# Kernel tuning notes

Measured on AMD Instinct MI355X. Metric: run time of the kernel, lower is better.

The kernel has to match this reference:

```python
import jax, jax.numpy as jnp
import numpy as np

N_LEVELS = 16
F_PER_LEVEL = 2
LOG2_T = 19
TABLE_SIZE = 1 << LOG2_T
BASE_RES = 16
MAX_RES = 4096
GEO_FEAT = 15
N_PTS = 524288

_b = np.exp((np.log(MAX_RES) - np.log(BASE_RES)) / (N_LEVELS - 1))
RES = np.floor(BASE_RES * _b ** np.arange(N_LEVELS)).astype(np.float32)  # [L]
PRIMES = np.array([1, 2654435761, 805459861], dtype=np.uint32)
# 8 trilinear corner offsets
OFFS = np.array([[(i >> 2) & 1, (i >> 1) & 1, i & 1] for i in range(8)], dtype=np.int32)


def hash_encode(x, table):
    # x: [N,3] in [0,1], table: [L,T,F]
    pos = x[None, :, :] * jnp.asarray(RES)[:, None, None]          # [L,N,3]
    p0 = jnp.floor(pos)
    frac = pos - p0                                                 # [L,N,3]
    corners = p0.astype(jnp.uint32)[:, :, None, :] + jnp.asarray(OFFS.astype(np.uint32))  # [L,N,8,3]
    hp = corners * jnp.asarray(PRIMES)                              # uint32 mul (wraps)
    h = (hp[..., 0] ^ hp[..., 1] ^ hp[..., 2]) & jnp.uint32(TABLE_SIZE - 1)  # [L,N,8]
    w = jnp.where(jnp.asarray(OFFS, bool), frac[:, :, None, :], 1.0 - frac[:, :, None, :]).prod(-1)  # [L,N,8]
    feats = jax.vmap(lambda t, i: t[i])(table, h)                   # [L,N,8,F] hashed gather
    out = (w[..., None] * feats).sum(axis=2)                        # [L,N,F]
    return out.transpose(1, 0, 2).reshape(x.shape[0], N_LEVELS * F_PER_LEVEL)  # [N,32]


def setup_inputs() -> dict:
    key = jax.random.key(0)
    ks = jax.random.split(key, 9)
    positions = jax.random.uniform(ks[0], (N_PTS, 3), dtype=jnp.float32)
    aabb = jnp.array([-1.0, -1.0, -1.0, 1.0, 1.0, 1.0], dtype=jnp.float32)
    table = jax.random.uniform(ks[1], (N_LEVELS, TABLE_SIZE, F_PER_LEVEL), minval=-1e-4, maxval=1e-4, dtype=jnp.float32)
    def lin(k, fan_in, fan_out):
        bound = 1.0 / np.sqrt(fan_in)
        kw, kb = jax.random.split(k)
        return (jax.random.uniform(kw, (fan_in, fan_out), minval=-bound, maxval=bound, dtype=jnp.float32),
                jax.random.uniform(kb, (fan_out,), minval=-bound, maxval=bound, dtype=jnp.float32))
    w1, b1 = lin(ks[2], 32, 64)
    w2, b2 = lin(ks[3], 64, 1 + GEO_FEAT)
    hw1, hb1 = lin(ks[4], GEO_FEAT, 64)
    hw2, hb2 = lin(ks[5], 64, 64)
    hw3, hb3 = lin(ks[6], 64, 3)
    return {"positions": positions, "aabb": aabb, "table": table,
            "w1": w1, "b1": b1, "w2": w2, "b2": b2,
            "hw1": hw1, "hb1": hb1, "hw2": hw2, "hb2": hb2, "hw3": hw3, "hb3": hb3}


def reference(positions, aabb, table, w1, b1, w2, b2, hw1, hb1, hw2, hb2, hw3, hb3):
    aabb_min, aabb_max = aabb[:3], aabb[3:]
    x = (positions - aabb_min) / (aabb_max - aabb_min)              # -> [0,1]
    selector = ((x > 0.0) & (x < 1.0)).all(axis=-1)                 # [N]
    enc = hash_encode(x, table)                                     # [N,32]
    h = jax.nn.relu(enc @ w1 + b1)                                  # [N,64]
    base = h @ w2 + b2                                              # [N,16]
    density_before = base[:, :1]
    embedding = base[:, 1:]
    density = jnp.exp(density_before - 1.0) * selector[:, None].astype(base.dtype)  # trunc_exp(x-1)
    hh = jax.nn.relu(embedding @ hw1 + hb1)
    hh = jax.nn.relu(hh @ hw2 + hb2)
    rgb = jax.nn.sigmoid(hh @ hw3 + hb3)                            # [N,3]
    return rgb, density
```

## Files before the change

kernel.cpp:

```cpp
#include <hip/hip_runtime.h>
#include <math.h>

#define NLV 16
#define TBLBITS 19
#define TBLMASK ((1u << TBLBITS) - 1u)
#define P2 2654435761u
#define P3 805459861u

#define D_BASE0 0
#define D_BASE1 4914
#define D_BASE2 18738
#define D_BASE3 58044
#define D_TOTAL 175694

typedef __attribute__((ext_vector_type(8))) short bf16x8;
typedef __attribute__((ext_vector_type(4))) float f32x4;

__device__ __forceinline__ unsigned f2bf(float f) {
    unsigned u = __builtin_bit_cast(unsigned, f);
    return (u + 0x7fffu + ((u >> 16) & 1u)) >> 16;
}

__global__ __launch_bounds__(256)
void dense_repack(const float* __restrict__ table, float* __restrict__ dense)
{
    const int i = blockIdx.x * 256 + threadIdx.x;
    if (i >= D_TOTAL) return;
    int g, lo, dim;
    if (i < 4913)                       { g = 0; lo = i;           dim = 17; }
    else if (i >= D_BASE1 && i < 18738) { g = 1; lo = i - D_BASE1; dim = 24; }
    else if (i >= D_BASE2 && i < 58042) { g = 2; lo = i - D_BASE2; dim = 34; }
    else if (i >= D_BASE3 && i < 175693){ g = 3; lo = i - D_BASE3; dim = 49; }
    else return;
    const unsigned z = (unsigned)lo % (unsigned)dim;
    const unsigned t = (unsigned)lo / (unsigned)dim;
    const unsigned y = t % (unsigned)dim;
    const unsigned x = t / (unsigned)dim;
    const unsigned h = (x ^ y * P2 ^ z * P3) & TBLMASK;
    const float* tl = table + ((size_t)g << 20);
    const float2 v = *reinterpret_cast<const float2*>(tl + ((size_t)h << 1));
    dense[(size_t)i * 2 + 0] = v.x;
    dense[(size_t)i * 2 + 1] = v.y;
}

__global__ __launch_bounds__(256)
void enc_kernel(const float* __restrict__ positions,
                const float* __restrict__ aabb,
                const float* __restrict__ table,
                unsigned* __restrict__ encOut, int npts,
                float r0_, float r1_, float r2_, float r3_,
                float r4_, float r5_, float r6_, float r7_,
                float r8_, float r9_, float r10_, float r11_,
                float r12_, float r13_, float r14_, float r15_)
{
    const unsigned l = blockIdx.y + 4u;
    const unsigned p = blockIdx.x * 256u + threadIdx.x;

    const bool s0 = (l & 1u), s1 = (l & 2u), s2 = (l & 4u), s3 = (l & 8u);
    float a0 = s0 ? r1_  : r0_;
    float a1 = s0 ? r3_  : r2_;
    float a2 = s0 ? r5_  : r4_;
    float a3 = s0 ? r7_  : r6_;
    float a4 = s0 ? r9_  : r8_;
    float a5 = s0 ? r11_ : r10_;
    float a6 = s0 ? r13_ : r12_;
    float a7 = s0 ? r15_ : r14_;
    float c0 = s1 ? a1 : a0;
    float c1 = s1 ? a3 : a2;
    float c2 = s1 ? a5 : a4;
    float c3 = s1 ? a7 : a6;
    float d0 = s2 ? c1 : c0;
    float d1 = s2 ? c3 : c2;
    const float r = s3 ? d1 : d0;

    const float px = positions[p * 3 + 0];
    const float py = positions[p * 3 + 1];
    const float pz = positions[p * 3 + 2];
    const float mnx = aabb[0], mny = aabb[1], mnz = aabb[2];
    const float mxx = aabb[3], mxy = aabb[4], mxz = aabb[5];
    const float x0 = (px - mnx) / (mxx - mnx);
    const float x1 = (py - mny) / (mxy - mny);
    const float x2 = (pz - mnz) / (mxz - mnz);

    const float fx = x0 * r, fy = x1 * r, fz = x2 * r;
    const float gx = floorf(fx), gy = floorf(fy), gz = floorf(fz);
    const unsigned cx = (unsigned)gx, cy = (unsigned)gy, cz = (unsigned)gz;
    const float rx = fx - gx, ry = fy - gy, rz = fz - gz;

    const float* tl = table + ((size_t)l << 20);
    float e0 = 0.f, e1 = 0.f;
    const bool xeven = (cx & 1u) == 0u;

    #pragma unroll
    for (int yz = 0; yz < 4; ++yz) {
        const unsigned dy = (yz >> 1) & 1, dz = yz & 1;
        const unsigned base = ((cy + dy) * P2) ^ ((cz + dz) * P3);
        const float wy = dy ? ry : 1.f - ry;
        const float wz = dz ? rz : 1.f - rz;
        const float wyz = wy * wz;
        const float wa = wyz * (1.f - rx);
        const float wb = wyz * rx;
        const unsigned i0 = (cx ^ base) & TBLMASK;

        float f0x, f0y, f1x, f1y;
        if (xeven) {
            const float4 q = *reinterpret_cast<const float4*>(
                tl + ((size_t)(i0 & ~1u) << 1));
            const bool lo = (i0 & 1u) == 0u;
            f0x = lo ? q.x : q.z;  f0y = lo ? q.y : q.w;
            f1x = lo ? q.z : q.x;  f1y = lo ? q.w : q.y;
        } else {
            const unsigned i1 = ((cx + 1u) ^ base) & TBLMASK;
            const float2 qa = *reinterpret_cast<const float2*>(tl + ((size_t)i0 << 1));
            const float2 qb = *reinterpret_cast<const float2*>(tl + ((size_t)i1 << 1));
            f0x = qa.x; f0y = qa.y; f1x = qb.x; f1y = qb.y;
        }
        e0 = fmaf(wa, f0x, e0); e0 = fmaf(wb, f1x, e0);
        e1 = fmaf(wa, f0y, e1); e1 = fmaf(wb, f1y, e1);
    }
    encOut[(size_t)(l - 4u) * npts + p] = f2bf(e0) | (f2bf(e1) << 16);
}

__global__ __launch_bounds__(256)
void prep_weights(const float* __restrict__ w1, const float* __restrict__ w2,
                  const float* __restrict__ hw1, const float* __restrict__ hw2,
                  const float* __restrict__ hw3, unsigned short* __restrict__ wt)
{
    const int i = blockIdx.x * 256 + threadIdx.x;
    if (i >= 12032) return;
    float v = 0.f;
    if (i < 2560) {
        int n = i / 40, k = i % 40;
        if (k < 32) v = w1[k * 64 + n];
    } else if (i < 5120) {
        int j = i - 2560, n = j / 40, k = j % 40;
        if (k < 15) v = hw1[k * 64 + n];
    } else if (i < 6272) {
        int j = i - 5120, n = j / 72, k = j % 72;
        if (k < 64) v = w2[k * 16 + n];
    } else if (i < 10880) {
        int j = i - 6272, n = j / 72, k = j % 72;
        if (k < 64) v = hw2[k * 64 + n];
    } else {
        int j = i - 10880, n = j / 72, k = j % 72;
        if (k < 64 && n < 3) v = hw3[k * 3 + n];
    }
    wt[i] = (unsigned short)f2bf(v);
}

__device__ __forceinline__ unsigned dense_gather(
    const float* __restrict__ dt, int g, float x0, float x1, float x2)
{
    const float r  = (g & 2) ? ((g & 1) ? 48.f : 33.f) : ((g & 1) ? 23.f : 16.f);
    const int  dim = (g & 2) ? ((g & 1) ? 49 : 34) : ((g & 1) ? 24 : 17);
    const int  bse = (g & 2) ? ((g & 1) ? D_BASE3 : D_BASE2)
                             : ((g & 1) ? D_BASE1 : D_BASE0);
    const float fx = x0 * r, fy = x1 * r, fz = x2 * r;
    const float gx = floorf(fx), gy = floorf(fy), gz = floorf(fz);
    const int cx = (int)gx, cy = (int)gy, cz = (int)gz;
    const float rx = fx - gx, ry = fy - gy, rz = fz - gz;
    float e0 = 0.f, e1 = 0.f;
    #pragma unroll
    for (int xy = 0; xy < 4; ++xy) {
        const int dx = xy >> 1, dy = xy & 1;
        const int row = ((cx + dx) * dim + (cy + dy)) * dim + cz + bse;
        const float wxy = (dx ? rx : 1.f - rx) * (dy ? ry : 1.f - ry);
        const float wa = wxy * (1.f - rz), wb = wxy * rz;
        float f0x, f0y, f1x, f1y;
        if (!(row & 1)) {
            const float4 q = *reinterpret_cast<const float4*>(dt + ((size_t)row << 1));
            f0x = q.x; f0y = q.y; f1x = q.z; f1y = q.w;
        } else {
            const float2 qa = *reinterpret_cast<const float2*>(dt + ((size_t)row << 1));
            const float2 qb = *reinterpret_cast<const float2*>(dt + ((size_t)(row + 1) << 1));
            f0x = qa.x; f0y = qa.y; f1x = qb.x; f1y = qb.y;
        }
        e0 = fmaf(wa, f0x, e0); e0 = fmaf(wb, f1x, e0);
        e1 = fmaf(wa, f0y, e1); e1 = fmaf(wb, f1y, e1);
    }
    return f2bf(e0) | (f2bf(e1) << 16);
}

__global__ __launch_bounds__(256)
void mlp_kernel(const unsigned* __restrict__ enc,
                const unsigned short* __restrict__ wt,
                const float* __restrict__ dense,
                const float* __restrict__ positions,
                const float* __restrict__ aabb,
                const float* __restrict__ b1, const float* __restrict__ b2,
                const float* __restrict__ hb1, const float* __restrict__ hb2,
                const float* __restrict__ hb3,
                float* __restrict__ out, int npts)
{
    __shared__ __align__(16) unsigned short H[4][32 * 72];
    __shared__ float sel_lds[128];

    const int tid  = threadIdx.x;
    const int wave = tid >> 6;
    const int lane = tid & 63;
    const int col  = lane & 15;
    const int lgrp = lane >> 4;
    const int blockPt = blockIdx.x * 128;
    const int wavePt  = blockPt + wave * 32;

    const float mnx = aabb[0], mny = aabb[1], mnz = aabb[2];
    const float mxx = aabb[3], mxy = aabb[4], mxz = aabb[5];

    if (lane < 32) {
        const int gp = wavePt + lane;
        const float px = positions[gp * 3 + 0];
        const float py = positions[gp * 3 + 1];
        const float pz = positions[gp * 3 + 2];
        const float x0 = (px - mnx) / (mxx - mnx);
        const float x1 = (py - mny) / (mxy - mny);
        const float x2 = (pz - mnz) / (mxz - mnz);
        const bool sel = (x0 > 0.f) && (x0 < 1.f) && (x1 > 0.f) && (x1 < 1.f) &&
                         (x2 > 0.f) && (x2 < 1.f);
        sel_lds[wave * 32 + lane] = sel ? 1.f : 0.f;
    }

    float bias1[4], biasH1[4], biasH2[4];
    #pragma unroll
    for (int nt = 0; nt < 4; ++nt) {
        bias1[nt]  = b1[nt * 16 + col];
        biasH1[nt] = hb1[nt * 16 + col];
        biasH2[nt] = hb2[nt * 16 + col];
    }
    const float bias2 = b2[col];
    const float biasH3 = (col < 3) ? hb3[col] : 0.f;

    bf16x8 a1[2];
    #pragma unroll
    for (int mt = 0; mt < 2; ++mt) {
        const int ptl = wavePt + mt * 16 + col;
        const float px = positions[ptl * 3 + 0];
        const float py = positions[ptl * 3 + 1];
        const float pz = positions[ptl * 3 + 2];
        const float x0 = (px - mnx) / (mxx - mnx);
        const float x1 = (py - mny) / (mxy - mny);
        const float x2 = (pz - mnz) / (mxz - mnz);
        const unsigned dv = dense_gather(dense, lgrp, x0, x1, x2);
        const int er = (lgrp == 0) ? 0 : (lgrp * 4 - 4);
        const unsigned e0v = enc[(size_t)(er + 0) * npts + ptl];
        const unsigned e1v = enc[(size_t)(er + 1) * npts + ptl];
        const unsigned e2v = enc[(size_t)(er + 2) * npts + ptl];
        const unsigned e3v = enc[(size_t)(er + 3) * npts + ptl];
        const int cbase = col * 4;
        const unsigned d0 = (unsigned)__builtin_amdgcn_ds_bpermute(cbase,       (int)dv);
        const unsigned d1 = (unsigned)__builtin_amdgcn_ds_bpermute(cbase + 64,  (int)dv);
        const unsigned d2 = (unsigned)__builtin_amdgcn_ds_bpermute(cbase + 128, (int)dv);
        const unsigned d3 = (unsigned)__builtin_amdgcn_ds_bpermute(cbase + 192, (int)dv);
        uint4 v;
        v.x = (lgrp == 0) ? d0 : e0v;
        v.y = (lgrp == 0) ? d1 : e1v;
        v.z = (lgrp == 0) ? d2 : e2v;
        v.w = (lgrp == 0) ? d3 : e3v;
        a1[mt] = __builtin_bit_cast(bf16x8, v);
    }

    const unsigned short* w1t = wt;
    const unsigned short* w3t = wt + 2560;
    const unsigned short* w2t = wt + 5120;
    const unsigned short* w4t = wt + 6272;
    const unsigned short* w5t = wt + 10880;
    unsigned short* Hw = H[wave];

    {
        f32x4 acc[2][4];
        #pragma unroll
        for (int mt = 0; mt < 2; ++mt)
            #pragma unroll
            for (int nt = 0; nt < 4; ++nt) {
                const float b = bias1[nt];
                acc[mt][nt] = (f32x4){b, b, b, b};
            }
        #pragma unroll
        for (int nt = 0; nt < 4; ++nt) {
            const bf16x8 b = *reinterpret_cast<const bf16x8*>(
                w1t + (nt * 16 + col) * 40 + lgrp * 8);
            #pragma unroll
            for (int mt = 0; mt < 2; ++mt)
                acc[mt][nt] = __builtin_amdgcn_mfma_f32_16x16x32_bf16(
                    a1[mt], b, acc[mt][nt], 0, 0, 0);
        }
        #pragma unroll
        for (int mt = 0; mt < 2; ++mt)
            #pragma unroll
            for (int nt = 0; nt < 4; ++nt)
                #pragma unroll
                for (int rr = 0; rr < 4; ++rr) {
                    const float h = fmaxf(acc[mt][nt][rr], 0.f);
                    const int row = mt * 16 + lgrp * 4 + rr;
                    Hw[row * 72 + nt * 16 + col] = (unsigned short)f2bf(h);
                }
    }

    {
        f32x4 acc[2];
        #pragma unroll
        for (int mt = 0; mt < 2; ++mt)
            acc[mt] = (f32x4){bias2, bias2, bias2, bias2};
        #pragma unroll
        for (int ks = 0; ks < 2; ++ks) {
            const bf16x8 b = *reinterpret_cast<const bf16x8*>(
                w2t + col * 72 + ks * 32 + lgrp * 8);
            #pragma unroll
            for (int mt = 0; mt < 2; ++mt) {
                const bf16x8 a = *reinterpret_cast<const bf16x8*>(
                    Hw + (mt * 16 + col) * 72 + ks * 32 + lgrp * 8);
                acc[mt] = __builtin_amdgcn_mfma_f32_16x16x32_bf16(
                    a, b, acc[mt], 0, 0, 0);
            }
        }
        #pragma unroll
        for (int mt = 0; mt < 2; ++mt)
            #pragma unroll
            for (int rr = 0; rr < 4; ++rr) {
                const float base = acc[mt][rr];
                const int row = mt * 16 + lgrp * 4 + rr;
                if (col == 0) {
                    const float dn = __expf(base - 1.f) * sel_lds[wave * 32 + row];
                    out[(size_t)npts * 3 + wavePt + row] = dn;
                } else {
                    Hw[row * 72 + (col - 1)] = (unsigned short)f2bf(base);
                }
            }
        if (lane < 32) {
            const int row = lane;
            Hw[row * 72 + 15] = 0;
            const uint4 z4 = {0, 0, 0, 0};
            *reinterpret_cast<uint4*>(Hw + row * 72 + 16) = z4;
            *reinterpret_cast<uint4*>(Hw + row * 72 + 24) = z4;
        }
    }

    {
        f32x4 acc[2][4];
        #pragma unroll
        for (int mt = 0; mt < 2; ++mt)
            #pragma unroll
            for (int nt = 0; nt < 4; ++nt) {
                const float b = biasH1[nt];
                acc[mt][nt] = (f32x4){b, b, b, b};
            }
        bf16x8 a[2];
        #pragma unroll
        for (int mt = 0; mt < 2; ++mt)
            a[mt] = *reinterpret_cast<const bf16x8*>(
                Hw + (mt * 16 + col) * 72 + lgrp * 8);
        #pragma unroll
        for (int nt = 0; nt < 4; ++nt) {
            const bf16x8 b = *reinterpret_cast<const bf16x8*>(
                w3t + (nt * 16 + col) * 40 + lgrp * 8);
            #pragma unroll
            for (int mt = 0; mt < 2; ++mt)
                acc[mt][nt] = __builtin_amdgcn_mfma_f32_16x16x32_bf16(
                    a[mt], b, acc[mt][nt], 0, 0, 0);
        }
        #pragma unroll
        for (int mt = 0; mt < 2; ++mt)
            #pragma unroll
            for (int nt = 0; nt < 4; ++nt)
                #pragma unroll
                for (int rr = 0; rr < 4; ++rr) {
                    const float h = fmaxf(acc[mt][nt][rr], 0.f);
                    const int row = mt * 16 + lgrp * 4 + rr;
                    Hw[row * 72 + nt * 16 + col] = (unsigned short)f2bf(h);
                }
    }

    {
        f32x4 acc[2][4];
        #pragma unroll
        for (int mt = 0; mt < 2; ++mt)
            #pragma unroll
            for (int nt = 0; nt < 4; ++nt) {
                const float b = biasH2[nt];
                acc[mt][nt] = (f32x4){b, b, b, b};
            }
        #pragma unroll
        for (int ks = 0; ks < 2; ++ks) {
            bf16x8 a[2];
            #pragma unroll
            for (int mt = 0; mt < 2; ++mt)
                a[mt] = *reinterpret_cast<const bf16x8*>(
                    Hw + (mt * 16 + col) * 72 + ks * 32 + lgrp * 8);
            #pragma unroll
            for (int nt = 0; nt < 4; ++nt) {
                const bf16x8 b = *reinterpret_cast<const bf16x8*>(
                    w4t + (nt * 16 + col) * 72 + ks * 32 + lgrp * 8);
                #pragma unroll
                for (int mt = 0; mt < 2; ++mt)
                    acc[mt][nt] = __builtin_amdgcn_mfma_f32_16x16x32_bf16(
                        a[mt], b, acc[mt][nt], 0, 0, 0);
            }
        }
        #pragma unroll
        for (int mt = 0; mt < 2; ++mt)
            #pragma unroll
            for (int nt = 0; nt < 4; ++nt)
                #pragma unroll
                for (int rr = 0; rr < 4; ++rr) {
                    const float h = fmaxf(acc[mt][nt][rr], 0.f);
                    const int row = mt * 16 + lgrp * 4 + rr;
                    Hw[row * 72 + nt * 16 + col] = (unsigned short)f2bf(h);
                }
    }

    {
        f32x4 acc[2];
        #pragma unroll
        for (int mt = 0; mt < 2; ++mt)
            acc[mt] = (f32x4){biasH3, biasH3, biasH3, biasH3};
        #pragma unroll
        for (int ks = 0; ks < 2; ++ks) {
            const bf16x8 b = *reinterpret_cast<const bf16x8*>(
                w5t + col * 72 + ks * 32 + lgrp * 8);
            #pragma unroll
            for (int mt = 0; mt < 2; ++mt) {
                const bf16x8 a = *reinterpret_cast<const bf16x8*>(
                    Hw + (mt * 16 + col) * 72 + ks * 32 + lgrp * 8);
                acc[mt] = __builtin_amdgcn_mfma_f32_16x16x32_bf16(
                    a, b, acc[mt], 0, 0, 0);
            }
        }
        if (col < 3) {
            #pragma unroll
            for (int mt = 0; mt < 2; ++mt)
                #pragma unroll
                for (int rr = 0; rr < 4; ++rr) {
                    const float v = acc[mt][rr];
                    const float rgb = 1.f / (1.f + __expf(-v));
                    const int row = mt * 16 + lgrp * 4 + rr;
                    out[(size_t)(wavePt + row) * 3 + col] = rgb;
                }
        }
    }
}

extern "C" void kernel_launch(void* const* d_in, const int* in_sizes, int n_in,
                              void* d_out, int out_size, void* d_ws, size_t ws_size,
                              hipStream_t stream) {
    const float* positions = (const float*)d_in[0];
    const float* aabb      = (const float*)d_in[1];
    const float* table     = (const float*)d_in[2];
    const float* w1  = (const float*)d_in[3];
    const float* b1  = (const float*)d_in[4];
    const float* w2  = (const float*)d_in[5];
    const float* b2  = (const float*)d_in[6];
    const float* hw1 = (const float*)d_in[7];
    const float* hb1 = (const float*)d_in[8];
    const float* hw2 = (const float*)d_in[9];
    const float* hb2 = (const float*)d_in[10];
    const float* hw3 = (const float*)d_in[11];
    const float* hb3 = (const float*)d_in[12];
    float* out = (float*)d_out;

    const int npts = in_sizes[0] / 3;

    unsigned* encbuf = (unsigned*)d_ws;
    unsigned short* wt = (unsigned short*)((char*)d_ws + (size_t)npts * 12 * 4);
    float* dense = (float*)((char*)d_ws + (size_t)npts * 12 * 4 + 24064);

    float R[NLV];
    const double bb = exp((log(4096.0) - log(16.0)) / 15.0);
    for (int l = 0; l < NLV; ++l)
        R[l] = (float)floor(16.0 * pow(bb, (double)l));

    prep_weights<<<47, 256, 0, stream>>>(w1, w2, hw1, hw2, hw3, wt);
    dense_repack<<<(D_TOTAL + 255) / 256, 256, 0, stream>>>(table, dense);

    dim3 egrid(npts / 256, 12);
    enc_kernel<<<egrid, 256, 0, stream>>>(
        positions, aabb, table, encbuf, npts,
        R[0], R[1], R[2], R[3], R[4], R[5], R[6], R[7],
        R[8], R[9], R[10], R[11], R[12], R[13], R[14], R[15]);

    mlp_kernel<<<npts / 128, 256, 0, stream>>>(
        encbuf, wt, dense, positions, aabb, b1, b2, hb1, hb2, hb3, out, npts);
}
```

Measured before the change: 327.4 us.

## Fuse hash-grid encoding into MLP kernel via shared-memory staging

Measured after the change: 447.5 us. +36.7%, slower.

```diff
diff --git a/kernel.cpp b/kernel.cpp
--- a/kernel.cpp
+++ b/kernel.cpp
@@ -15,6 +15,8 @@
 
 typedef __attribute__((ext_vector_type(8))) short bf16x8;
 typedef __attribute__((ext_vector_type(4))) float f32x4;
+
+struct ResArr { float r[NLV]; };
 
 __device__ __forceinline__ unsigned f2bf(float f) {
     unsigned u = __builtin_bit_cast(unsigned, f);
@@ -41,84 +43,6 @@
     const float2 v = *reinterpret_cast<const float2*>(tl + ((size_t)h << 1));
     dense[(size_t)i * 2 + 0] = v.x;
     dense[(size_t)i * 2 + 1] = v.y;
-}
-
-__global__ __launch_bounds__(256)
-void enc_kernel(const float* __restrict__ positions,
-                const float* __restrict__ aabb,
-                const float* __restrict__ table,
-                unsigned* __restrict__ encOut, int npts,
-                float r0_, float r1_, float r2_, float r3_,
-                float r4_, float r5_, float r6_, float r7_,
-                float r8_, float r9_, float r10_, float r11_,
-                float r12_, float r13_, float r14_, float r15_)
-{
-    const unsigned l = blockIdx.y + 4u;
-    const unsigned p = blockIdx.x * 256u + threadIdx.x;
-
-    const bool s0 = (l & 1u), s1 = (l & 2u), s2 = (l & 4u), s3 = (l & 8u);
-    float a0 = s0 ? r1_  : r0_;
-    float a1 = s0 ? r3_  : r2_;
-    float a2 = s0 ? r5_  : r4_;
-    float a3 = s0 ? r7_  : r6_;
-    float a4 = s0 ? r9_  : r8_;
-    float a5 = s0 ? r11_ : r10_;
-    float a6 = s0 ? r13_ : r12_;
-    float a7 = s0 ? r15_ : r14_;
-    float c0 = s1 ? a1 : a0;
-    float c1 = s1 ? a3 : a2;
-    float c2 = s1 ? a5 : a4;
-    float c3 = s1 ? a7 : a6;
-    float d0 = s2 ? c1 : c0;
-    float d1 = s2 ? c3 : c2;
-    const float r = s3 ? d1 : d0;
-
-    const float px = positions[p * 3 + 0];
-    const float py = positions[p * 3 + 1];
-    const float pz = positions[p * 3 + 2];
-    const float mnx = aabb[0], mny = aabb[1], mnz = aabb[2];
-    const float mxx = aabb[3], mxy = aabb[4], mxz = aabb[5];
-    const float x0 = (px - mnx) / (mxx - mnx);
-    const float x1 = (py - mny) / (mxy - mny);
-    const float x2 = (pz - mnz) / (mxz - mnz);
-
-    const float fx = x0 * r, fy = x1 * r, fz = x2 * r;
-    const float gx = floorf(fx), gy = floorf(fy), gz = floorf(fz);
-    const unsigned cx = (unsigned)gx, cy = (unsigned)gy, cz = (unsigned)gz;
-    const float rx = fx - gx, ry = fy - gy, rz = fz - gz;
-
-    const float* tl = table + ((size_t)l << 20);
-    float e0 = 0.f, e1 = 0.f;
-    const bool xeven = (cx & 1u) == 0u;
-
-    #pragma unroll
-    for (int yz = 0; yz < 4; ++yz) {
-        const unsigned dy = (yz >> 1) & 1, dz = yz & 1;
-        const unsigned base = ((cy + dy) * P2) ^ ((cz + dz) * P3);
-        const float wy = dy ? ry : 1.f - ry;
-        const float wz = dz ? rz : 1.f - rz;
-        const float wyz = wy * wz;
-        const float wa = wyz * (1.f - rx);
-        const float wb = wyz * rx;
-        const unsigned i0 = (cx ^ base) & TBLMASK;
-
-        float f0x, f0y, f1x, f1y;
-        if (xeven) {
-            const float4 q = *reinterpret_cast<const float4*>(
-                tl + ((size_t)(i0 & ~1u) << 1));
-            const bool lo = (i0 & 1u) == 0u;
-            f0x = lo ? q.x : q.z;  f0y = lo ? q.y : q.w;
-            f1x = lo ? q.z : q.x;  f1y = lo ? q.w : q.y;
-        } else {
-            const unsigned i1 = ((cx + 1u) ^ base) & TBLMASK;
-            const float2 qa = *reinterpret_cast<const float2*>(tl + ((size_t)i0 << 1));
-            const float2 qb = *reinterpret_cast<const float2*>(tl + ((size_t)i1 << 1));
-            f0x = qa.x; f0y = qa.y; f1x = qb.x; f1y = qb.y;
-        }
-        e0 = fmaf(wa, f0x, e0); e0 = fmaf(wb, f1x, e0);
-        e1 = fmaf(wa, f0y, e1); e1 = fmaf(wb, f1y, e1);
-    }
-    encOut[(size_t)(l - 4u) * npts + p] = f2bf(e0) | (f2bf(e1) << 16);
 }
 
 __global__ __launch_bounds__(256)
@@ -181,17 +105,18 @@
     return f2bf(e0) | (f2bf(e1) << 16);
 }
 
-__global__ __launch_bounds__(256)
-void mlp_kernel(const unsigned* __restrict__ enc,
-                const unsigned short* __restrict__ wt,
-                const float* __restrict__ dense,
-                const float* __restrict__ positions,
-                const float* __restrict__ aabb,
-                const float* __restrict__ b1, const float* __restrict__ b2,
-                const float* __restrict__ hb1, const float* __restrict__ hb2,
-                const float* __restrict__ hb3,
-                float* __restrict__ out, int npts)
+__global__ __launch_bounds__(256, 4)
+void fused_kernel(const float* __restrict__ positions,
+                  const float* __restrict__ aabb,
+                  const float* __restrict__ table,
+                  const float* __restrict__ dense,
+                  const unsigned short* __restrict__ wt,
+                  const float* __restrict__ b1, const float* __restrict__ b2,
+                  const float* __restrict__ hb1, const float* __restrict__ hb2,
+                  const float* __restrict__ hb3,
+                  float* __restrict__ out, int npts, ResArr R)
 {
+    __shared__ unsigned enc_s[128 * 17];
     __shared__ __align__(16) unsigned short H[4][32 * 72];
     __shared__ float sel_lds[128];
 
@@ -206,18 +131,71 @@
     const float mnx = aabb[0], mny = aabb[1], mnz = aabb[2];
     const float mxx = aabb[3], mxy = aabb[4], mxz = aabb[5];
 
-    if (lane < 32) {
-        const int gp = wavePt + lane;
-        const float px = positions[gp * 3 + 0];
-        const float py = positions[gp * 3 + 1];
-        const float pz = positions[gp * 3 + 2];
+    {
+        const int mypt = tid & 127;
+        const int h = tid >> 7;
+        const float px = positions[(blockPt + mypt) * 3 + 0];
+        const float py = positions[(blockPt + mypt) * 3 + 1];
+        const float pz = positions[(blockPt + mypt) * 3 + 2];
         const float x0 = (px - mnx) / (mxx - mnx);
         const float x1 = (py - mny) / (mxy - mny);
         const float x2 = (pz - mnz) / (mxz - mnz);
-        const bool sel = (x0 > 0.f) && (x0 < 1.f) && (x1 > 0.f) && (x1 < 1.f) &&
-                         (x2 > 0.f) && (x2 < 1.f);
-        sel_lds[wave * 32 + lane] = sel ? 1.f : 0.f;
-    }
+
+        if (h == 0) {
+            const bool sel = (x0 > 0.f) && (x0 < 1.f) && (x1 > 0.f) &&
+                             (x1 < 1.f) && (x2 > 0.f) && (x2 < 1.f);
+            sel_lds[mypt] = sel ? 1.f : 0.f;
+        }
+
+        #pragma unroll
+        for (int j = 0; j < 8; ++j) {
+            unsigned dv;
+            if (j < 2) {
+                dv = dense_gather(dense, 2 * j + h, x0, x1, x2);
+            } else {
+                const float r = h ? R.r[2 * j + 1] : R.r[2 * j];
+                const float fx = x0 * r, fy = x1 * r, fz = x2 * r;
+                const float gx = floorf(fx), gy = floorf(fy), gz = floorf(fz);
+                const unsigned cx = (unsigned)gx, cy = (unsigned)gy, cz = (unsigned)gz;
+                const float rx = fx - gx, ry = fy - gy, rz = fz - gz;
+                const float* tl = table + ((size_t)(2 * j + h) << 20);
+                float e0 = 0.f, e1 = 0.f;
+                const bool xeven = (cx & 1u) == 0u;
+                #pragma unroll
+                for (int yz = 0; yz < 4; ++yz) {
+                    const unsigned dy = (yz >> 1) & 1, dz = yz & 1;
+                    const unsigned base = ((cy + dy) * P2) ^ ((cz + dz) * P3);
+                    const float wy = dy ? ry : 1.f - ry;
+                    const float wz = dz ? rz : 1.f - rz;
+                    const float wyz = wy * wz;
+                    const float wa = wyz * (1.f - rx);
+                    const float wb = wyz * rx;
+                    const unsigned i0 = (cx ^ base) & TBLMASK;
+                    float f0x, f0y, f1x, f1y;
+                    if (xeven) {
+                        const float4 q = *reinterpret_cast<const float4*>(
+                            tl + ((size_t)(i0 & ~1u) << 1));
+                        const bool lo = (i0 & 1u) == 0u;
+                        f0x = lo ? q.x : q.z;  f0y = lo ? q.y : q.w;
+                        f1x = lo ? q.z : q.x;  f1y = lo ? q.w : q.y;
+                    } else {
+                        const unsigned i1 = ((cx + 1u) ^ base) & TBLMASK;
+                        const float2 qa = *reinterpret_cast<const float2*>(
+                            tl + ((size_t)i0 << 1));
+                        const float2 qb = *reinterpret_cast<const float2*>(
+                            tl + ((size_t)i1 << 1));
+                        f0x = qa.x; f0y = qa.y; f1x = qb.x; f1y = qb.y;
+                    }
+                    e0 = fmaf(wa, f0x, e0); e0 = fmaf(wb, f1x, e0);
+                    e1 = fmaf(wa, f0y, e1); e1 = fmaf(wb, f1y, e1);
+                }
+                dv = f2bf(e0) | (f2bf(e1) << 16);
+            }
+            enc_s[mypt * 17 + 2 * j + h] = dv;
+        }
+    }
+
+    __syncthreads();
 
     float bias1[4], biasH1[4], biasH2[4];
     #pragma unroll
@@ -232,29 +210,12 @@
     bf16x8 a1[2];
     #pragma unroll
     for (int mt = 0; mt < 2; ++mt) {
-        const int ptl = wavePt + mt * 16 + col;
-        const float px = positions[ptl * 3 + 0];
-        const float py = positions[ptl * 3 + 1];
-        const float pz = positions[ptl * 3 + 2];
-        const float x0 = (px - mnx) / (mxx - mnx);
-        const float x1 = (py - mny) / (mxy - mny);
-        const float x2 = (pz - mnz) / (mxz - mnz);
-        const unsigned dv = dense_gather(dense, lgrp, x0, x1, x2);
-        const int er = (lgrp == 0) ? 0 : (lgrp * 4 - 4);
-        const unsigned e0v = enc[(size_t)(er + 0) * npts + ptl];
-        const unsigned e1v = enc[(size_t)(er + 1) * npts + ptl];
-        const unsigned e2v = enc[(size_t)(er + 2) * npts + ptl];
-        const unsigned e3v = enc[(size_t)(er + 3) * npts + ptl];
-        const int cbase = col * 4;
-        const unsigned d0 = (unsigned)__builtin_amdgcn_ds_bpermute(cbase,       (int)dv);
-        const unsigned d1 = (unsigned)__builtin_amdgcn_ds_bpermute(cbase + 64,  (int)dv);
-        const unsigned d2 = (unsigned)__builtin_amdgcn_ds_bpermute(cbase + 128, (int)dv);
-        const unsigned d3 = (unsigned)__builtin_amdgcn_ds_bpermute(cbase + 192, (int)dv);
+        const int ptl = wave * 32 + mt * 16 + col;
         uint4 v;
-        v.x = (lgrp == 0) ? d0 : e0v;
-        v.y = (lgrp == 0) ? d1 : e1v;
-        v.z = (lgrp == 0) ? d2 : e2v;
-        v.w = (lgrp == 0) ? d3 : e3v;
+        v.x = enc_s[ptl * 17 + lgrp * 4 + 0];
+        v.y = enc_s[ptl * 17 + lgrp * 4 + 1];
+        v.z = enc_s[ptl * 17 + lgrp * 4 + 2];
+        v.w = enc_s[ptl * 17 + lgrp * 4 + 3];
         a1[mt] = __builtin_bit_cast(bf16x8, v);
     }
 
@@ -458,24 +419,18 @@
 
     const int npts = in_sizes[0] / 3;
 
-    unsigned* encbuf = (unsigned*)d_ws;
-    unsigned short* wt = (unsigned short*)((char*)d_ws + (size_t)npts * 12 * 4);
-    float* dense = (float*)((char*)d_ws + (size_t)npts * 12 * 4 + 24064);
-
-    float R[NLV];
+    unsigned short* wt = (unsigned short*)d_ws;
+    float* dense = (float*)((char*)d_ws + 24064);
+
+    ResArr R;
     const double bb = exp((log(4096.0) - log(16.0)) / 15.0);
     for (int l = 0; l < NLV; ++l)
-        R[l] = (float)floor(16.0 * pow(bb, (double)l));
+        R.r[l] = (float)floor(16.0 * pow(bb, (double)l));
 
     prep_weights<<<47, 256, 0, stream>>>(w1, w2, hw1, hw2, hw3, wt);
     dense_repack<<<(D_TOTAL + 255) / 256, 256, 0, stream>>>(table, dense);
 
-    dim3 egrid(npts / 256, 12);
-    enc_kernel<<<egrid, 256, 0, stream>>>(
-        positions, aabb, table, encbuf, npts,
-        R[0], R[1], R[2], R[3], R[4], R[5], R[6], R[7],
-        R[8], R[9], R[10], R[11], R[12], R[13], R[14], R[15]);
-
-    mlp_kernel<<<npts / 128, 256, 0, stream>>>(
-        encbuf, wt, dense, positions, aabb, b1, b2, hb1, hb2, hb3, out, npts);
-}
+    fused_kernel<<<npts / 128, 256, 0, stream>>>(
+        positions, aabb, table, dense, wt,
+        b1, b2, hb1, hb2, hb3, out, npts, R);
+}
```

## Pipeline encoding and MLP across point chunks in mixed software-pipelined kernel

Applied to the files above, without the earlier changes.

New measurement: 414.7 us. 26.7% more time.

```diff
diff --git a/kernel.cpp b/kernel.cpp
--- a/kernel.cpp
+++ b/kernel.cpp
@@ -12,6 +12,10 @@
 #define D_BASE2 18738
 #define D_BASE3 58044
 #define D_TOTAL 175694
+
+#define WT_OFF    0
+#define DENSE_OFF 24064
+#define ENC_OFF   1429632
 
 typedef __attribute__((ext_vector_type(8))) short bf16x8;
 typedef __attribute__((ext_vector_type(4))) float f32x4;
@@ -41,84 +45,6 @@
     const float2 v = *reinterpret_cast<const float2*>(tl + ((size_t)h << 1));
     dense[(size_t)i * 2 + 0] = v.x;
     dense[(size_t)i * 2 + 1] = v.y;
-}
-
-__global__ __launch_bounds__(256)
-void enc_kernel(const float* __restrict__ positions,
-                const float* __restrict__ aabb,
-                const float* __restrict__ table,
-                unsigned* __restrict__ encOut, int npts,
-                float r0_, float r1_, float r2_, float r3_,
-                float r4_, float r5_, float r6_, float r7_,
-                float r8_, float r9_, float r10_, float r11_,
-                float r12_, float r13_, float r14_, float r15_)
-{
-    const unsigned l = blockIdx.y + 4u;
-    const unsigned p = blockIdx.x * 256u + threadIdx.x;
-
-    const bool s0 = (l & 1u), s1 = (l & 2u), s2 = (l & 4u), s3 = (l & 8u);
-    float a0 = s0 ? r1_  : r0_;
-    float a1 = s0 ? r3_  : r2_;
-    float a2 = s0 ? r5_  : r4_;
-    float a3 = s0 ? r7_  : r6_;
-    float a4 = s0 ? r9_  : r8_;
-    float a5 = s0 ? r11_ : r10_;
-    float a6 = s0 ? r13_ : r12_;
-    float a7 = s0 ? r15_ : r14_;
-    float c0 = s1 ? a1 : a0;
-    float c1 = s1 ? a3 : a2;
-    float c2 = s1 ? a5 : a4;
-    float c3 = s1 ? a7 : a6;
-    float d0 = s2 ? c1 : c0;
-    float d1 = s2 ? c3 : c2;
-    const float r = s3 ? d1 : d0;
-
-    const float px = positions[p * 3 + 0];
-    const float py = positions[p * 3 + 1];
-    const float pz = positions[p * 3 + 2];
-    const float mnx = aabb[0], mny = aabb[1], mnz = aabb[2];
-    const float mxx = aabb[3], mxy = aabb[4], mxz = aabb[5];
-    const float x0 = (px - mnx) / (mxx - mnx);
-    const float x1 = (py - mny) / (mxy - mny);
-    const float x2 = (pz - mnz) / (mxz - mnz);
-
-    const float fx = x0 * r, fy = x1 * r, fz = x2 * r;
-    const float gx = floorf(fx), gy = floorf(fy), gz = floorf(fz);
-    const unsigned cx = (unsigned)gx, cy = (unsigned)gy, cz = (unsigned)gz;
-    const float rx = fx - gx, ry = fy - gy, rz = fz - gz;
-
-    const float* tl = table + ((size_t)l << 20);
-    float e0 = 0.f, e1 = 0.f;
-    const bool xeven = (cx & 1u) == 0u;
-
-    #pragma unroll
-    for (int yz = 0; yz < 4; ++yz) {
-        const unsigned dy = (yz >> 1) & 1, dz = yz & 1;
-        const unsigned base = ((cy + dy) * P2) ^ ((cz + dz) * P3);
-        const float wy = dy ? ry : 1.f - ry;
-        const float wz = dz ? rz : 1.f - rz;
-        const float wyz = wy * wz;
-        const float wa = wyz * (1.f - rx);
-        const float wb = wyz * rx;
-        const unsigned i0 = (cx ^ base) & TBLMASK;
-
-        float f0x, f0y, f1x, f1y;
-        if (xeven) {
-            const float4 q = *reinterpret_cast<const float4*>(
-                tl + ((size_t)(i0 & ~1u) << 1));
-            const bool lo = (i0 & 1u) == 0u;
-            f0x = lo ? q.x : q.z;  f0y = lo ? q.y : q.w;
-            f1x = lo ? q.z : q.x;  f1y = lo ? q.w : q.y;
-        } else {
-            const unsigned i1 = ((cx + 1u) ^ base) & TBLMASK;
-            const float2 qa = *reinterpret_cast<const float2*>(tl + ((size_t)i0 << 1));
-            const float2 qb = *reinterpret_cast<const float2*>(tl + ((size_t)i1 << 1));
-            f0x = qa.x; f0y = qa.y; f1x = qb.x; f1y = qb.y;
-        }
-        e0 = fmaf(wa, f0x, e0); e0 = fmaf(wb, f1x, e0);
-        e1 = fmaf(wa, f0y, e1); e1 = fmaf(wb, f1y, e1);
-    }
-    encOut[(size_t)(l - 4u) * npts + p] = f2bf(e0) | (f2bf(e1) << 16);
 }
 
 __global__ __launch_bounds__(256)
@@ -182,29 +108,118 @@
 }
 
 __global__ __launch_bounds__(256)
-void mlp_kernel(const unsigned* __restrict__ enc,
-                const unsigned short* __restrict__ wt,
-                const float* __restrict__ dense,
-                const float* __restrict__ positions,
-                const float* __restrict__ aabb,
-                const float* __restrict__ b1, const float* __restrict__ b2,
-                const float* __restrict__ hb1, const float* __restrict__ hb2,
-                const float* __restrict__ hb3,
-                float* __restrict__ out, int npts)
+void mixed_kernel(const float* __restrict__ positions,
+                  const float* __restrict__ aabb,
+                  const float* __restrict__ table,
+                  const float* __restrict__ dense,
+                  const unsigned short* __restrict__ wt,
+                  unsigned* __restrict__ encbuf,
+                  const float* __restrict__ b1, const float* __restrict__ b2,
+                  const float* __restrict__ hb1, const float* __restrict__ hb2,
+                  const float* __restrict__ hb3,
+                  float* __restrict__ out, int npts,
+                  int encBase, int encPts, int mlpBase, int mlpPts,
+                  float r0_, float r1_, float r2_, float r3_,
+                  float r4_, float r5_, float r6_, float r7_,
+                  float r8_, float r9_, float r10_, float r11_,
+                  float r12_, float r13_, float r14_, float r15_)
 {
     __shared__ __align__(16) unsigned short H[4][32 * 72];
     __shared__ float sel_lds[128];
 
+    const unsigned G  = ((unsigned)encPts >> 8) << 4;
+    const unsigned M  = (unsigned)mlpPts >> 7;
+    const unsigned nT = G + M;
+    const unsigned bid = blockIdx.x;
+    const unsigned mB = (unsigned)(((unsigned long long)bid * M) / nT);
+    const unsigned mA = (unsigned)(((unsigned long long)(bid + 1) * M) / nT);
+
     const int tid  = threadIdx.x;
+    const float mnx = aabb[0], mny = aabb[1], mnz = aabb[2];
+    const float mxx = aabb[3], mxy = aabb[4], mxz = aabb[5];
+
+    if (mA == mB) {
+        const unsigned g = bid - mB;
+        const unsigned perLvl = (unsigned)encPts >> 8;
+        const unsigned lvl = g / perLvl;
+        const unsigned chunk = g - lvl * perLvl;
+        const int p = encBase + (int)(chunk * 256u) + tid;
+
+        const bool s0 = (lvl & 1u), s1 = (lvl & 2u), s2 = (lvl & 4u), s3 = (lvl & 8u);
+        float a0 = s0 ? r1_  : r0_;
+        float a1 = s0 ? r3_  : r2_;
+        float a2 = s0 ? r5_  : r4_;
+        float a3 = s0 ? r7_  : r6_;
+        float a4 = s0 ? r9_  : r8_;
+        float a5 = s0 ? r11_ : r10_;
+        float a6 = s0 ? r13_ : r12_;
+        float a7 = s0 ? r15_ : r14_;
+        float c0 = s1 ? a1 : a0;
+        float c1 = s1 ? a3 : a2;
+        float c2 = s1 ? a5 : a4;
+        float c3 = s1 ? a7 : a6;
+        float d0 = s2 ? c1 : c0;
+        float d1 = s2 ? c3 : c2;
+        const float r = s3 ? d1 : d0;
+
+        const float px = positions[p * 3 + 0];
+        const float py = positions[p * 3 + 1];
+        const float pz = positions[p * 3 + 2];
+        const float x0 = (px - mnx) / (mxx - mnx);
+        const float x1 = (py - mny) / (mxy - mny);
+        const float x2 = (pz - mnz) / (mxz - mnz);
+
+        unsigned dv;
+        if (lvl < 4u) {
+            dv = dense_gather(dense, (int)lvl, x0, x1, x2);
+        } else {
+            const float fx = x0 * r, fy = x1 * r, fz = x2 * r;
+            const float gx = floorf(fx), gy = floorf(fy), gz = floorf(fz);
+            const unsigned cx = (unsigned)gx, cy = (unsigned)gy, cz = (unsigned)gz;
+            const float rx = fx - gx, ry = fy - gy, rz = fz - gz;
+            const float* tl = table + ((size_t)lvl << 20);
+            float e0 = 0.f, e1 = 0.f;
+            const bool xeven = (cx & 1u) == 0u;
+            #pragma unroll
+            for (int yz = 0; yz < 4; ++yz) {
+                const unsigned dy = (yz >> 1) & 1, dz = yz & 1;
+                const unsigned base = ((cy + dy) * P2) ^ ((cz + dz) * P3);
+                const float wy = dy ? ry : 1.f - ry;
+                const float wz = dz ? rz : 1.f - rz;
+                const float wyz = wy * wz;
+                const float wa = wyz * (1.f - rx);
+                const float wb = wyz * rx;
+                const unsigned i0 = (cx ^ base) & TBLMASK;
+                float f0x, f0y, f1x, f1y;
+                if (xeven) {
+                    const float4 q = *reinterpret_cast<const float4*>(
+                        tl + ((size_t)(i0 & ~1u) << 1));
+                    const bool lo = (i0 & 1u) == 0u;
+                    f0x = lo ? q.x : q.z;  f0y = lo ? q.y : q.w;
+                    f1x = lo ? q.z : q.x;  f1y = lo ? q.w : q.y;
+                } else {
+                    const unsigned i1 = ((cx + 1u) ^ base) & TBLMASK;
+                    const float2 qa = *reinterpret_cast<const float2*>(
+                        tl + ((size_t)i0 << 1));
+                    const float2 qb = *reinterpret_cast<const float2*>(
+                        tl + ((size_t)i1 << 1));
+                    f0x = qa.x; f0y = qa.y; f1x = qb.x; f1y = qb.y;
+                }
+                e0 = fmaf(wa, f0x, e0); e0 = fmaf(wb, f1x, e0);
+                e1 = fmaf(wa, f0y, e1); e1 = fmaf(wb, f1y, e1);
+            }
+            dv = f2bf(e0) | (f2bf(e1) << 16);
+        }
+        encbuf[(size_t)lvl * npts + p] = dv;
+        return;
+    }
+
     const int wave = tid >> 6;
     const int lane = tid & 63;
     const int col  = lane & 15;
     const int lgrp = lane >> 4;
-    const int blockPt = blockIdx.x * 128;
+    const int blockPt = mlpBase + (int)mB * 128;
     const int wavePt  = blockPt + wave * 32;
-
-    const float mnx = aabb[0], mny = aabb[1], mnz = aabb[2];
-    const float mxx = aabb[3], mxy = aabb[4], mxz = aabb[5];
 
     if (lane < 32) {
         const int gp = wavePt + lane;
@@ -233,28 +248,11 @@
     #pragma unroll
     for (int mt = 0; mt < 2; ++mt) {
         const int ptl = wavePt + mt * 16 + col;
-        const float px = positions[ptl * 3 + 0];
-        const float py = positions[ptl * 3 + 1];
-        const float pz = positions[ptl * 3 + 2];
-        const float x0 = (px - mnx) / (mxx - mnx);
-        const float x1 = (py - mny) / (mxy - mny);
-        const float x2 = (pz - mnz) / (mxz - mnz);
-        const unsigned dv = dense_gather(dense, lgrp, x0, x1, x2);
-        const int er = (lgrp == 0) ? 0 : (lgrp * 4 - 4);
-        const unsigned e0v = enc[(size_t)(er + 0) * npts + ptl];
-        const unsigned e1v = enc[(size_t)(er + 1) * npts + ptl];
-        const unsigned e2v = enc[(size_t)(er + 2) * npts + ptl];
-        const unsigned e3v = enc[(size_t)(er + 3) * npts + ptl];
-        const int cbase = col * 4;
-        const unsigned d0 = (unsigned)__builtin_amdgcn_ds_bpermute(cbase,       (int)dv);
-        const unsigned d1 = (unsigned)__builtin_amdgcn_ds_bpermute(cbase + 64,  (int)dv);
-        const unsigned d2 = (unsigned)__builtin_amdgcn_ds_bpermute(cbase + 128, (int)dv);
-        const unsigned d3 = (unsigned)__builtin_amdgcn_ds_bpermute(cbase + 192, (int)dv);
         uint4 v;
-        v.x = (lgrp == 0) ? d0 : e0v;
-        v.y = (lgrp == 0) ? d1 : e1v;
-        v.z = (lgrp == 0) ? d2 : e2v;
-        v.w = (lgrp == 0) ? d3 : e3v;
+        v.x = encbuf[(size_t)(lgrp * 4 + 0) * npts + ptl];
+        v.y = encbuf[(size_t)(lgrp * 4 + 1) * npts + ptl];
+        v.z = encbuf[(size_t)(lgrp * 4 + 2) * npts + ptl];
+        v.w = encbuf[(size_t)(lgrp * 4 + 3) * npts + ptl];
         a1[mt] = __builtin_bit_cast(bf16x8, v);
     }
 
@@ -294,7 +292,6 @@
                     Hw[row * 72 + nt * 16 + col] = (unsigned short)f2bf(h);
                 }
     }
-
     {
         f32x4 acc[2];
         #pragma unroll
@@ -333,7 +330,6 @@
             *reinterpret_cast<uint4*>(Hw + row * 72 + 24) = z4;
         }
     }
-
     {
         f32x4 acc[2][4];
         #pragma unroll
@@ -368,7 +364,6 @@
                     Hw[row * 72 + nt * 16 + col] = (unsigned short)f2bf(h);
                 }
     }
-
     {
         f32x4 acc[2][4];
         #pragma unroll
@@ -406,7 +401,6 @@
                     Hw[row * 72 + nt * 16 + col] = (unsigned short)f2bf(h);
                 }
     }
-
     {
         f32x4 acc[2];
         #pragma unroll
@@ -458,9 +452,9 @@
 
     const int npts = in_sizes[0] / 3;
 
-    unsigned* encbuf = (unsigned*)d_ws;
-    unsigned short* wt = (unsigned short*)((char*)d_ws + (size_t)npts * 12 * 4);
-    float* dense = (float*)((char*)d_ws + (size_t)npts * 12 * 4 + 24064);
+    unsigned short* wt = (unsigned short*)((char*)d_ws + WT_OFF);
+    float* dense       = (float*)((char*)d_ws + DENSE_OFF);
+    unsigned* encbuf   = (unsigned*)((char*)d_ws + ENC_OFF);
 
     float R[NLV];
     const double bb = exp((log(4096.0) - log(16.0)) / 15.0);
@@ -470,12 +464,22 @@
     prep_weights<<<47, 256, 0, stream>>>(w1, w2, hw1, hw2, hw3, wt);
     dense_repack<<<(D_TOTAL + 255) / 256, 256, 0, stream>>>(table, dense);
 
-    dim3 egrid(npts / 256, 12);
-    enc_kernel<<<egrid, 256, 0, stream>>>(
-        positions, aabb, table, encbuf, npts,
-        R[0], R[1], R[2], R[3], R[4], R[5], R[6], R[7],
-        R[8], R[9], R[10], R[11], R[12], R[13], R[14], R[15]);
-
-    mlp_kernel<<<npts / 128, 256, 0, stream>>>(
-        encbuf, wt, dense, positions, aabb, b1, b2, hb1, hb2, hb3, out, npts);
-}
+    const int sz[5]   = {167936, 126976, 94208, 73728, 61440};
+    int base[5];
+    base[0] = 0;
+    for (int i = 1; i < 5; ++i) base[i] = base[i - 1] + sz[i - 1];
+
+    for (int s = 0; s <= 5; ++s) {
+        const int encPts = (s <= 4) ? sz[s] : 0;
+        const int encB   = (s <= 4) ? base[s] : 0;
+        const int mlpPts = (s >= 1) ? sz[s - 1] : 0;
+        const int mlpB   = (s >= 1) ? base[s - 1] : 0;
+        const int nT = (encPts / 256) * 16 + mlpPts / 128;
+        mixed_kernel<<<nT, 256, 0, stream>>>(
+            positions, aabb, table, dense, wt, encbuf,
+            b1, b2, hb1, hb2, hb3, out, npts,
+            encB, encPts, mlpB, mlpPts,
+            R[0], R[1], R[2], R[3], R[4], R[5], R[6], R[7],
+            R[8], R[9], R[10], R[11], R[12], R[13], R[14], R[15]);
+    }
+}
```
